# Kernel tuning notes

Hardware: AMD Instinct MI355X
Metric: run time of the kernel (lower is better)

## Reference

```python
import jax, jax.numpy as jnp
import numpy as np

HORIZON = 15
LAT = 6
CIN = 48  # input_dim // horizon
EPS = 1e-5
PAD = (HORIZON - 1) // 2  # 7


def _conv1d(x, w, b):
    # x: [B, Cin, L], w: [Cout, Cin, K], 'same' padding (pad=7, K=15)
    y = jax.lax.conv_general_dilated(
        x, w, window_strides=(1,), padding=[(PAD, PAD)],
        dimension_numbers=('NCH', 'OIH', 'NCH'))
    return y + b[None, :, None]


def _bn_ncl(x, g, b):
    # BatchNorm1d train-mode on [N, C, L]: stats over (N, L), biased var
    m = jnp.mean(x, axis=(0, 2), keepdims=True)
    v = jnp.mean(jnp.square(x - m), axis=(0, 2), keepdims=True)
    return (x - m) * jax.lax.rsqrt(v + EPS) * g[None, :, None] + b[None, :, None]


def setup_inputs() -> dict:
    key = jax.random.key(0)
    ks = jax.random.split(key, 16)
    B = 65536
    s1 = 1.0 / np.sqrt(CIN * HORIZON)
    s2 = 1.0 / np.sqrt(CIN * HORIZON)
    s3 = 1.0 / np.sqrt(2 * LAT * HORIZON)
    sp = 1.0 / np.sqrt(HORIZON)
    return {
        'x':  jax.random.normal(ks[0], (B, CIN * HORIZON), jnp.float32),
        'w1': jax.random.normal(ks[1], (CIN, CIN, HORIZON), jnp.float32) * s1,
        'b1': jax.random.normal(ks[2], (CIN,), jnp.float32) * s1,
        'g1': jnp.ones((CIN,), jnp.float32),
        'be1': jnp.zeros((CIN,), jnp.float32),
        'w2': jax.random.normal(ks[3], (2 * LAT, CIN, HORIZON), jnp.float32) * s2,
        'b2': jax.random.normal(ks[4], (2 * LAT,), jnp.float32) * s2,
        'g2': jnp.ones((2 * LAT,), jnp.float32),
        'be2': jnp.zeros((2 * LAT,), jnp.float32),
        'w3': jax.random.normal(ks[5], (LAT, 2 * LAT, HORIZON), jnp.float32) * s3,
        'b3': jax.random.normal(ks[6], (LAT,), jnp.float32) * s3,
        'pw': jax.random.normal(ks[7], (LAT, 2, HORIZON), jnp.float32) * sp,
        'pb': jax.random.normal(ks[8], (LAT, 2), jnp.float32) * sp,
        'pg': jnp.ones((LAT, 2), jnp.float32),
        'pbe': jnp.zeros((LAT, 2), jnp.float32),
    }


def reference(x, w1, b1, g1, be1, w2, b2, g2, be2, w3, b3, pw, pb, pg, pbe):
    B = x.shape[0]
    h = x.reshape(B, CIN, HORIZON)
    h = jax.nn.elu(_bn_ncl(_conv1d(h, w1, b1), g1, be1))
    h = jax.nn.elu(_bn_ncl(_conv1d(h, w2, b2), g2, be2))
    h = _conv1d(h, w3, b3)  # [B, LAT, HORIZON]

    # FFT spectral stats over last dim (length 15 -> 8 rfft bins)
    rf = jnp.fft.rfft(h, axis=2)
    power = jnp.square(jnp.abs(rf[:, :, 1:]))  # drop DC, [B, LAT, 7]
    freqs = jnp.arange(1, HORIZON // 2 + 1, dtype=h.dtype)  # rfftfreq(15)[1:]*15
    psum = jnp.sum(power, axis=2)
    f = jnp.sum(freqs * power, axis=2) / psum
    a = 2.0 * jnp.sqrt(psum) / HORIZON
    b_off = jnp.real(rf[:, :, 0]) / HORIZON

    # per-channel phase encoder, vectorized: Linear(15->2) + BatchNorm1d(2)
    v = jnp.einsum('bcl,col->bco', h, pw) + pb  # [B, LAT, 2]
    m = jnp.mean(v, axis=0, keepdims=True)
    var = jnp.mean(jnp.square(v - m), axis=0, keepdims=True)
    v = (v - m) * jax.lax.rsqrt(var + EPS) * pg + pbe
    p = jnp.arctan2(v[..., 1], v[..., 0]) / (2.0 * np.pi)  # [B, LAT]

    return jnp.concatenate([p, f, a, b_off], axis=-1)  # [B, 4*LAT]
```

## Files before the change

### kernel.cpp

```cpp
#include <hip/hip_runtime.h>
#include <math.h>

#define HORIZON 15
#define PAD 7
#define CIN 48
#define C2 12
#define LAT 6
#define EPS 1e-5f
#define NREP 16

typedef __bf16 bf16x8 __attribute__((ext_vector_type(8)));
typedef float f32x4 __attribute__((ext_vector_type(4)));
typedef unsigned short ushort8v __attribute__((ext_vector_type(8)));
typedef unsigned short ushortT;

__device__ inline void bfsplit(float v, ushortT& h, ushortT& l) {
    __bf16 bh = (__bf16)v;
    float fh = (float)bh;
    __bf16 bl = (__bf16)(v - fh);
    h = __builtin_bit_cast(ushortT, bh);
    l = __builtin_bit_cast(ushortT, bl);
}

__global__ void prep_kernel(const float* __restrict__ w1, const float* __restrict__ w2,
                            const float* __restrict__ w3,
                            ushortT* __restrict__ w1h, ushortT* __restrict__ w1l,
                            ushortT* __restrict__ w2h, ushortT* __restrict__ w2l,
                            float* __restrict__ w3t, float* __restrict__ trig) {
    int idx = blockIdx.x * blockDim.x + threadIdx.x;
    const int n1 = 768 * 736;
    const int n2 = 256 * 736;
    const int n3 = C2 * HORIZON * LAT;
    if (idx < n1) {
        int n = idx / 736, k = idx % 736;
        float v = 0.f;
        if (n < 720 && k < 720) {
            int l = n / 48, co = n % 48, ci = k / 15, t = k % 15;
            int d = t - l;
            if (d >= -PAD && d <= PAD) v = w1[(co * CIN + ci) * HORIZON + (d + PAD)];
        }
        ushortT h, lo; bfsplit(v, h, lo);
        w1h[idx] = h; w1l[idx] = lo;
    } else if (idx < n1 + n2) {
        int j = idx - n1;
        int n = j / 736, k = j % 736;
        float v = 0.f;
        if (n < 180 && k < 720) {
            int l = n / 12, co = n % 12, t = k / 48, ci = k % 48;
            int d = t - l;
            if (d >= -PAD && d <= PAD) v = w2[(co * CIN + ci) * HORIZON + (d + PAD)];
        }
        ushortT h, lo; bfsplit(v, h, lo);
        w2h[j] = h; w2l[j] = lo;
    } else if (idx < n1 + n2 + n3) {
        int j = idx - n1 - n2;
        int co = j % LAT; int r = j / LAT; int k = r % HORIZON; int ci = r / HORIZON;
        w3t[j] = w3[(co * C2 + ci) * HORIZON + k];
    } else if (idx < n1 + n2 + n3 + 7 * HORIZON) {
        int j = idx - (n1 + n2 + n3);
        int l = j % HORIZON; int f = j / HORIZON + 1;
        double ang = -2.0 * 3.14159265358979323846 * (double)(f * l) / 15.0;
        trig[j * 2]     = (float)cos(ang);
        trig[j * 2 + 1] = (float)sin(ang);
    }
}

#define SBAR() asm volatile("s_barrier" ::: "memory")
#define GLDS16(SRC, DST)                                                      \
    __builtin_amdgcn_global_load_lds(                                         \
        (const __attribute__((address_space(1))) void*)(SRC),                 \
        (__attribute__((address_space(3))) void*)(DST), 16, 0, 0)

template <int NFRAG, int CSTAT, bool FUSE_BN, int NCG>
__global__ __launch_bounds__(256, 3)
void gemm_split(const float* __restrict__ A, int Ka,
                const ushortT* __restrict__ Bh, const ushortT* __restrict__ Bl,
                const float* __restrict__ bnp,
                float* __restrict__ Y, int ldy, int nreal,
                float* __restrict__ stats) {
    constexpr int NB  = 8;
    constexpr int NBW = NB / 4;
    constexpr int NVM = NBW * 2 + 4;

    __shared__ __attribute__((aligned(16))) ushortT s_bh[2][NB * 512];
    __shared__ __attribute__((aligned(16))) ushortT s_bl[2][NB * 512];
    __shared__ float s_stats[2 * CSTAT];
    __shared__ float s_bnp[96];

    const int tid = threadIdx.x;
    const int w = tid >> 6, lane = tid & 63;
    const int lr = lane & 15, lq = lane >> 4;
    if (tid < 2 * CSTAT) s_stats[tid] = 0.f;
    if (FUSE_BN && tid < 96) s_bnp[tid] = bnp[tid];
    __syncthreads();

    const int bid = blockIdx.x;
    const int xcd = bid & 7, s = bid >> 3;
    const int rpx = (gridDim.x >> 3) / NCG;
    const int col = s % NCG;
    const int rowblk = xcd * rpx + s / NCG;
    const long m_base = (long)rowblk * 128;
    const int n0 = col * (NFRAG * 16);

    const float* arow0 = A + (m_base + w * 32 + lr) * (long)Ka;
    const float* arow1 = arow0 + 16 * (long)Ka;
    const long bdelta = Bl - Bh;
    const ushortT* bsrc[NBW];
#pragma unroll
    for (int j = 0; j < NBW; j++)
        bsrc[j] = Bh + (long)(n0 + (w * NBW + j) * 16 + lr) * 736 + lq * 8;

    f32x4 acc[2][NFRAG];
#pragma unroll
    for (int i = 0; i < 2; i++)
#pragma unroll
        for (int jf = 0; jf < NFRAG; jf++) acc[i][jf] = (f32x4){0.f, 0.f, 0.f, 0.f};

    float4 pfA[4], pfB[4];
    bf16x8 ah[2], al[2];

#define ISSUE_STEP(KS, BUF, PF)                                               \
    do {                                                                      \
        const int k0_ = (KS) * 32;                                            \
        _Pragma("unroll")                                                     \
        for (int j_ = 0; j_ < NBW; j_++) {                                    \
            const ushortT* g_ = bsrc[j_] + k0_;                               \
            GLDS16(g_, &s_bh[BUF][(w * NBW + j_) * 512]);                     \
            GLDS16(g_ + bdelta, &s_bl[BUF][(w * NBW + j_) * 512]);            \
        }                                                                     \
        const int ka_ = k0_ + lq * 8;                                         \
        _Pragma("unroll")                                                     \
        for (int fr_ = 0; fr_ < 2; fr_++) {                                   \
            float4 z_ = make_float4(0.f, 0.f, 0.f, 0.f);                      \
            PF[fr_ * 2] = z_; PF[fr_ * 2 + 1] = z_;                           \
            if (ka_ < Ka) {                                                   \
                const float4* p_ =                                            \
                    (const float4*)((fr_ ? arow1 : arow0) + ka_);             \
                PF[fr_ * 2] = p_[0]; PF[fr_ * 2 + 1] = p_[1];                 \
            }                                                                 \
        }                                                                     \
    } while (0)

#define SPLIT_STEP(PF, KS)                                                    \
    do {                                                                      \
        const int kb_ = (KS) * 32 + lq * 8;                                   \
        float4 qq_[4];                                                        \
        if (FUSE_BN) {                                                        \
            const int cb_ = (kb_ % 48) * 2;       \
            _Pragma("unroll")                                                 \
            for (int m_ = 0; m_ < 4; m_++)                                    \
                qq_[m_] = *(const float4*)(&s_bnp[cb_ + m_ * 4]);             \
        }                                                                     \
        _Pragma("unroll")                                                     \
        for (int fr_ = 0; fr_ < 2; fr_++) {                                   \
            float f_[8] = {PF[fr_*2].x,   PF[fr_*2].y,                        \
                           PF[fr_*2].z,   PF[fr_*2].w,                        \
                           PF[fr_*2+1].x, PF[fr_*2+1].y,                      \
                           PF[fr_*2+1].z, PF[fr_*2+1].w};                     \
            ushort8v uh_, ul_;                                                \
            _Pragma("unroll")                                                 \
            for (int jj = 0; jj < 8; jj++) {                                  \
                float v_ = f_[jj];                                            \
                if (FUSE_BN) {                                                \
                    float sc_ = (jj & 1) ? qq_[jj >> 1].z : qq_[jj >> 1].x;   \
                    float sh_ = (jj & 1) ? qq_[jj >> 1].w : qq_[jj >> 1].y;   \
                    float h_ = fmaf(v_, sc_, sh_);                            \
                    v_ = h_ > 0.f ? h_ : expm1f(h_);                          \
                }                                                             \
                ushortT hh_, ll_; bfsplit(v_, hh_, ll_);                      \
                uh_[jj] = hh_; ul_[jj] = ll_;                                 \
            }                                                                 \
            ah[fr_] = __builtin_bit_cast(bf16x8, uh_);                        \
            al[fr_] = __builtin_bit_cast(bf16x8, ul_);                        \
        }                                                                     \
    } while (0)

#define COMPUTE_STEP(BUF)                                                     \
    do {                                                                      \
        __builtin_amdgcn_s_setprio(1);                                        \
        _Pragma("unroll")                                                     \
        for (int fc = 0; fc < NFRAG; fc++) {                                  \
            bf16x8 bhf = *(const bf16x8*)(&s_bh[BUF][fc * 512 + lane * 8]);   \
            bf16x8 blf = *(const bf16x8*)(&s_bl[BUF][fc * 512 + lane * 8]);   \
            _Pragma("unroll")                                                 \
            for (int fr = 0; fr < 2; fr++) {                                  \
                acc[fr][fc] = __builtin_amdgcn_mfma_f32_16x16x32_bf16(        \
                    ah[fr], bhf, acc[fr][fc], 0, 0, 0);                       \
                acc[fr][fc] = __builtin_amdgcn_mfma_f32_16x16x32_bf16(        \
                    al[fr], bhf, acc[fr][fc], 0, 0, 0);                       \
                acc[fr][fc] = __builtin_amdgcn_mfma_f32_16x16x32_bf16(        \
                    ah[fr], blf, acc[fr][fc], 0, 0, 0);                       \
            }                                                                 \
        }                                                                     \
        __builtin_amdgcn_s_setprio(0);                                        \
    } while (0)

#define WAITP() asm volatile("s_waitcnt vmcnt(%0)" ::"n"(NVM) : "memory")

    ISSUE_STEP(0, 0, pfA);
#pragma unroll 1
    for (int k2 = 0; k2 + 2 < 23; k2 += 2) {
        ISSUE_STEP(k2 + 1, 1, pfB);
        WAITP();
        SBAR();
        SPLIT_STEP(pfA, k2);
        COMPUTE_STEP(0);
        SBAR();
        ISSUE_STEP(k2 + 2, 0, pfA);
        WAITP();
        SBAR();
        SPLIT_STEP(pfB, k2 + 1);
        COMPUTE_STEP(1);
        SBAR();
    }
    asm volatile("s_waitcnt vmcnt(0)" ::: "memory");
    SBAR();
    SPLIT_STEP(pfA, 22);
    COMPUTE_STEP(0);

#undef ISSUE_STEP
#undef SPLIT_STEP
#undef COMPUTE_STEP
#undef WAITP

    float ps[3] = {0.f, 0.f, 0.f}, qs[3] = {0.f, 0.f, 0.f};
#pragma unroll
    for (int fc = 0; fc < NFRAG; fc++) {
        int colY = n0 + fc * 16 + lr;
        int j = fc % 3;
#pragma unroll
        for (int fr = 0; fr < 2; fr++) {
#pragma unroll
            for (int r = 0; r < 4; r++) {
                float v = acc[fr][fc][r];
                long row = m_base + w * 32 + fr * 16 + lq * 4 + r;
                if (colY < nreal) Y[row * (long)ldy + colY] = v;
                ps[j] += v;
                qs[j] = fmaf(v, v, qs[j]);
            }
        }
    }
#pragma unroll
    for (int j = 0; j < 3; j++) {
        int c = (n0 + lr + 16 * j) % CSTAT;
        atomicAdd(&s_stats[c], ps[j]);
        atomicAdd(&s_stats[CSTAT + c], qs[j]);
    }
    __syncthreads();
    if (tid < 2 * CSTAT)
        atomicAdd(&stats[(rowblk & (NREP - 1)) * 2 * CSTAT + tid], s_stats[tid]);
}

__global__ void finalize_bn(const float* __restrict__ stats, const float* __restrict__ g,
                            const float* __restrict__ be, float* __restrict__ bn,
                            int C, float invN) {
    int c = threadIdx.x;
    if (c >= C) return;
    float s1 = 0.f, s2 = 0.f;
    for (int r = 0; r < NREP; r++) { s1 += stats[r * 2 * C + c]; s2 += stats[r * 2 * C + C + c]; }
    float m   = s1 * invN;
    float var = s2 * invN - m * m;
    float sc  = g[c] * rsqrtf(var + EPS);
    bn[c * 2]     = sc;
    bn[c * 2 + 1] = fmaf(-m, sc, be[c]);
}

__global__ __launch_bounds__(256) void tail_kernel(const float* __restrict__ h2,
                                                   const float* __restrict__ w3t,
                                                   const float* __restrict__ b3,
                                                   const float* __restrict__ pw,
                                                   const float* __restrict__ trig,
                                                   const float* __restrict__ bn2,
                                                   float* __restrict__ out,
                                                   float* __restrict__ vout,
                                                   float* __restrict__ stats) {
    __shared__ float s_sum[2 * LAT];
    __shared__ float s_sq[2 * LAT];
    int t = threadIdx.x;
    if (t < 2 * LAT) { s_sum[t] = 0.f; s_sq[t] = 0.f; }
    __syncthreads();

    int id = blockIdx.x * 256 + t;
    int co = id % LAT;
    long b = id / LAT;
    const float* xr = h2 + b * (long)(C2 * HORIZON);

    float acc[HORIZON];
#pragma unroll
    for (int l = 0; l < HORIZON; l++) acc[l] = b3[co];

    for (int ci = 0; ci < C2; ci++) {
        float sc = bn2[ci * 2], sh = bn2[ci * 2 + 1];
        float xv[HORIZON];
#pragma unroll
        for (int tt = 0; tt < HORIZON; tt++) {
            float h = fmaf(xr[tt * C2 + ci], sc, sh);
            xv[tt] = h > 0.f ? h : expm1f(h);
        }
        float wv[HORIZON];
#pragma unroll
        for (int k = 0; k < HORIZON; k++) wv[k] = w3t[(ci * HORIZON + k) * LAT + co];
#pragma unroll
        for (int tt = 0; tt < HORIZON; tt++) {
            const int lo = (tt - PAD) > 0 ? (tt - PAD) : 0;
            const int hi = (tt + PAD) < (HORIZON - 1) ? (tt + PAD) : (HORIZON - 1);
#pragma unroll
            for (int l = lo; l <= hi; l++)
                acc[l] = fmaf(xv[tt], wv[tt - l + PAD], acc[l]);
        }
    }

    float ssum = 0.f;
#pragma unroll
    for (int l = 0; l < HORIZON; l++) ssum += acc[l];
    float b_off = ssum * (1.f / 15.f);

    float psum = 0.f, fnum = 0.f;
#pragma unroll
    for (int j = 0; j < 7; j++) {
        float re = 0.f, im = 0.f;
#pragma unroll
        for (int l = 0; l < HORIZON; l++) {
            float c = trig[(j * HORIZON + l) * 2];
            float s = trig[(j * HORIZON + l) * 2 + 1];
            re = fmaf(acc[l], c, re);
            im = fmaf(acc[l], s, im);
        }
        float p = fmaf(re, re, im * im);
        psum += p;
        fnum = fmaf((float)(j + 1), p, fnum);
    }
    float f = fnum / psum;
    float a = 2.f * sqrtf(psum) * (1.f / 15.f);

    float* orow = out + b * 24;
    orow[6 + co]  = f;
    orow[12 + co] = a;
    orow[18 + co] = b_off;

    float v0 = 0.f, v1 = 0.f;
#pragma unroll
    for (int l = 0; l < HORIZON; l++) {
        v0 = fmaf(acc[l], pw[(co * 2 + 0) * HORIZON + l], v0);
        v1 = fmaf(acc[l], pw[(co * 2 + 1) * HORIZON + l], v1);
    }
    vout[b * 12 + co * 2]     = v0;
    vout[b * 12 + co * 2 + 1] = v1;
    atomicAdd(&s_sum[co * 2], v0);
    atomicAdd(&s_sq[co * 2], v0 * v0);
    atomicAdd(&s_sum[co * 2 + 1], v1);
    atomicAdd(&s_sq[co * 2 + 1], v1 * v1);

    __syncthreads();
    float* st = stats + (blockIdx.x & (NREP - 1)) * 2 * (2 * LAT);
    if (t < 2 * LAT) {
        atomicAdd(&st[t], s_sum[t]);
        atomicAdd(&st[2 * LAT + t], s_sq[t]);
    }
}

__global__ void phase_kernel(const float* __restrict__ v, const float* __restrict__ bnP,
                             float* __restrict__ out, long B) {
    long b = (long)blockIdx.x * 256 + threadIdx.x;
    if (b >= B) return;
#pragma unroll
    for (int co = 0; co < LAT; co++) {
        float v0 = v[b * 12 + co * 2];
        float v1 = v[b * 12 + co * 2 + 1];
        int c0 = co * 2, c1 = co * 2 + 1;
        v0 = fmaf(v0, bnP[c0 * 2], bnP[c0 * 2 + 1]);
        v1 = fmaf(v1, bnP[c1 * 2], bnP[c1 * 2 + 1]);
        out[b * 24 + co] = atan2f(v1, v0) * 0.15915494309189535f;
    }
}

extern "C" void kernel_launch(void* const* d_in, const int* in_sizes, int n_in,
                              void* d_out, int out_size, void* d_ws, size_t ws_size,
                              hipStream_t stream) {
    const float* x   = (const float*)d_in[0];
    const float* w1  = (const float*)d_in[1];
    const float* g1  = (const float*)d_in[3];
    const float* be1 = (const float*)d_in[4];
    const float* w2  = (const float*)d_in[5];
    const float* g2  = (const float*)d_in[7];
    const float* be2 = (const float*)d_in[8];
    const float* w3  = (const float*)d_in[9];
    const float* b3  = (const float*)d_in[10];
    const float* pw  = (const float*)d_in[11];
    const float* pg  = (const float*)d_in[13];
    const float* pbe = (const float*)d_in[14];
    float* out = (float*)d_out;

    long B = (long)in_sizes[0] / (CIN * HORIZON);

    ushortT* w1h = (ushortT*)d_ws;
    ushortT* w1l = w1h + 768 * 736;
    ushortT* w2h = w1l + 768 * 736;
    ushortT* w2l = w2h + 256 * 736;
    float* y1 = (float*)(w2l + 256 * 736);
    float* y2 = y1 + B * 720;
    float* vv = y2 + B * 180;
    float* stats1 = vv + B * 12;
    float* stats2 = stats1 + NREP * 96;
    float* statsP = stats2 + NREP * 24;
    float* bn1 = statsP + NREP * 24;
    float* bn2 = bn1 + 96;
    float* bnP = bn2 + 24;
    float* w3t = bnP + 24;
    float* trig = w3t + C2 * HORIZON * LAT;

    hipMemsetAsync(stats1, 0, NREP * (96 + 24 + 24) * sizeof(float), stream);

    const int prep_total = 768 * 736 + 256 * 736 + C2 * HORIZON * LAT + 7 * HORIZON;
    prep_kernel<<<(prep_total + 255) / 256, 256, 0, stream>>>(w1, w2, w3, w1h, w1l, w2h, w2l, w3t, trig);

    gemm_split<8, 48, false, 6><<<3072, 256, 0, stream>>>(
        x, 720, w1h, w1l, nullptr, y1, 720, 720, stats1);
    finalize_bn<<<1, 64, 0, stream>>>(stats1, g1, be1, bn1, CIN, 1.f / (float)(B * HORIZON));

    gemm_split<6, 12, true, 2><<<1024, 256, 0, stream>>>(
        y1, 720, w2h, w2l, bn1, y2, 180, 180, stats2);
    finalize_bn<<<1, 64, 0, stream>>>(stats2, g2, be2, bn2, C2, 1.f / (float)(B * HORIZON));

    tail_kernel<<<(int)(B * LAT / 256), 256, 0, stream>>>(y2, w3t, b3, pw, trig, bn2, out, vv, statsP);
    finalize_bn<<<1, 64, 0, stream>>>(statsP, pg, pbe, bnP, 2 * LAT, 1.f / (float)B);

    phase_kernel<<<(int)((B + 255) / 256), 256, 0, stream>>>(vv, bnP, out, B);
}
```

Measured before the change: 782.4 us.

## Deepen GEMM prefetch pipeline from double to triple buffering

The split-bf16 GEMM loop moves from two LDS/register stages to three. Two K-steps of B tiles (via global_load_lds) and A float4 prefetches are now in flight while the current step is split and computed, with explicit vmcnt waits. The goal is to hide more global-load latency behind MFMA work. The cost is 50% more LDS per block and more prefetch registers, which could cut occupancy under launch_bounds(256,3). The hardcoded vmcnt values (24, 12) may not match the real number of loads per step, which risks racing on unfinished loads.

```diff
diff --git a/kernel.cpp b/kernel.cpp
--- a/kernel.cpp
+++ b/kernel.cpp
@@ -66,6 +66,7 @@
 }
 
 #define SBAR() asm volatile("s_barrier" ::: "memory")
+#define WAITN(N) asm volatile("s_waitcnt vmcnt(" #N ")" ::: "memory")
 #define GLDS16(SRC, DST)                                                      \
     __builtin_amdgcn_global_load_lds(                                         \
         (const __attribute__((address_space(1))) void*)(SRC),                 \
@@ -80,10 +81,9 @@
                 float* __restrict__ stats) {
     constexpr int NB  = 8;
     constexpr int NBW = NB / 4;
-    constexpr int NVM = NBW * 2 + 4;
-
-    __shared__ __attribute__((aligned(16))) ushortT s_bh[2][NB * 512];
-    __shared__ __attribute__((aligned(16))) ushortT s_bl[2][NB * 512];
+
+    __shared__ __attribute__((aligned(16))) ushortT s_bh[3][NB * 512];
+    __shared__ __attribute__((aligned(16))) ushortT s_bl[3][NB * 512];
     __shared__ float s_stats[2 * CSTAT];
     __shared__ float s_bnp[96];
 
@@ -116,7 +116,7 @@
 #pragma unroll
         for (int jf = 0; jf < NFRAG; jf++) acc[i][jf] = (f32x4){0.f, 0.f, 0.f, 0.f};
 
-    float4 pfA[4], pfB[4];
+    float4 pf0[4], pf1[4], pf2[4];
     bf16x8 ah[2], al[2];
 
 #define ISSUE_STEP(KS, BUF, PF)                                               \
@@ -195,33 +195,28 @@
         __builtin_amdgcn_s_setprio(0);                                        \
     } while (0)
 
-#define WAITP() asm volatile("s_waitcnt vmcnt(%0)" ::"n"(NVM) : "memory")
-
-    ISSUE_STEP(0, 0, pfA);
+    ISSUE_STEP(0, 0, pf0);
+    ISSUE_STEP(1, 1, pf1);
 #pragma unroll 1
-    for (int k2 = 0; k2 + 2 < 23; k2 += 2) {
-        ISSUE_STEP(k2 + 1, 1, pfB);
-        WAITP();
-        SBAR();
-        SPLIT_STEP(pfA, k2);
-        COMPUTE_STEP(0);
-        SBAR();
-        ISSUE_STEP(k2 + 2, 0, pfA);
-        WAITP();
-        SBAR();
-        SPLIT_STEP(pfB, k2 + 1);
-        COMPUTE_STEP(1);
-        SBAR();
-    }
-    asm volatile("s_waitcnt vmcnt(0)" ::: "memory");
-    SBAR();
-    SPLIT_STEP(pfA, 22);
-    COMPUTE_STEP(0);
+    for (int j3 = 0; j3 <= 18; j3 += 3) {
+        ISSUE_STEP(j3 + 2, 2, pf2);
+        WAITN(24); SBAR();
+        SPLIT_STEP(pf0, j3);     COMPUTE_STEP(0); SBAR();
+        ISSUE_STEP(j3 + 3, 0, pf0);
+        WAITN(24); SBAR();
+        SPLIT_STEP(pf1, j3 + 1); COMPUTE_STEP(1); SBAR();
+        ISSUE_STEP(j3 + 4, 1, pf1);
+        WAITN(24); SBAR();
+        SPLIT_STEP(pf2, j3 + 2); COMPUTE_STEP(2); SBAR();
+    }
+    WAITN(12); SBAR();
+    SPLIT_STEP(pf0, 21); COMPUTE_STEP(0); SBAR();
+    WAITN(0);  SBAR();
+    SPLIT_STEP(pf1, 22); COMPUTE_STEP(1);
 
 #undef ISSUE_STEP
 #undef SPLIT_STEP
 #undef COMPUTE_STEP
-#undef WAITP
 
     float ps[3] = {0.f, 0.f, 0.f}, qs[3] = {0.f, 0.f, 0.f};
 #pragma unroll
```

After: 790.8 us. About the same (+1.1%).
